# Kernel tuning notes

Measured on AMD Instinct MI355X. Metric: run time of the kernel, lower is better.

The kernel has to match this reference:

```python
import jax, jax.numpy as jnp
import numpy as np

G, NPG, K = 128, 1024, 16          # graphs, nodes per graph, kNN neighbors
NB_IN = 3
SLOPE = 0.01                        # torch.nn.LeakyReLU default negative_slope


def leaky(v):
    return jnp.where(v >= 0, v, SLOPE * v)


def knn_idx(pos, k):
    """pos: [G, n, 3] -> neighbor indices [G, n, k] within each graph, self excluded.
    Matches torch_geometric.nn.knn_graph (k nearest by Euclidean distance)."""
    sq = jnp.sum(pos * pos, axis=-1)                              # [G, n]
    d2 = sq[:, :, None] + sq[:, None, :] - 2.0 * jnp.einsum('gnd,gmd->gnm', pos, pos)
    n = pos.shape[1]
    d2 = d2 + jnp.eye(n, dtype=pos.dtype) * 1e9                   # exclude self-loops
    _, idx = jax.lax.top_k(-d2, k)                                # k smallest distances
    return idx


def edge_conv(h, idx, W1, b1, W2, b2):
    """EdgeConv with aggr='add': sum_j mlp(cat([x_i, x_j - x_i])).
    h: [G, n, F], idx: [G, n, k] -> [G, n, out]"""
    xj = jax.vmap(lambda hg, ig: hg[ig])(h, idx)                  # gather: [G, n, k, F]
    xi = jnp.broadcast_to(h[:, :, None, :], xj.shape)
    m = jnp.concatenate([xi, xj - xi], axis=-1)                   # [G, n, k, 2F]
    m = leaky(m @ W1 + b1)
    m = leaky(m @ W2 + b2)
    return jnp.sum(m, axis=2)                                     # scatter-add over k


def _linear_init(key, fin, fout):
    kw, kb = jax.random.split(key)
    lim = 1.0 / np.sqrt(fin)
    W = jax.random.uniform(kw, (fin, fout), jnp.float32, -lim, lim)
    b = jax.random.uniform(kb, (fout,), jnp.float32, -lim, lim)
    return W, b


def setup_inputs() -> dict:
    key = jax.random.key(0)
    ks = jax.random.split(key, 10)
    x = jax.random.normal(ks[0], (G * NPG, NB_IN), jnp.float32)
    batch = jnp.repeat(jnp.arange(G, dtype=jnp.int32), NPG)
    # layer 1 MLP: [2*3 -> 16 -> 16]; layer 2 MLP: [2*16 -> 16 -> 16]
    W1a, b1a = _linear_init(ks[1], 2 * NB_IN, 16)
    W2a, b2a = _linear_init(ks[2], 16, 16)
    W1b, b1b = _linear_init(ks[3], 2 * 16, 16)
    W2b, b2b = _linear_init(ks[4], 16, 16)
    # post-processing: [3+16+16=35 -> 16 -> 16]
    Wp1, bp1 = _linear_init(ks[5], 35, 16)
    Wp2, bp2 = _linear_init(ks[6], 16, 16)
    # readout: [16*3 poolings = 48 -> 128 -> 10]
    Wr1, br1 = _linear_init(ks[7], 48, 128)
    Wr2, br2 = _linear_init(ks[8], 128, 10)
    return {"x": x, "batch": batch,
            "W1a": W1a, "b1a": b1a, "W2a": W2a, "b2a": b2a,
            "W1b": W1b, "b1b": b1b, "W2b": W2b, "b2b": b2b,
            "Wp1": Wp1, "bp1": bp1, "Wp2": Wp2, "bp2": bp2,
            "Wr1": Wr1, "br1": br1, "Wr2": Wr2, "br2": br2}


def reference(x, batch, W1a, b1a, W2a, b2a, W1b, b1b, W2b, b2b,
              Wp1, bp1, Wp2, bp2, Wr1, br1, Wr2, br2):
    # equal-sized graphs sorted by batch id -> reshape to [G, n, F]
    h = x.reshape(G, NPG, -1)
    skips = [h]
    for (W1, b1, W2, b2) in ((W1a, b1a, W2a, b2a), (W1b, b1b, W2b, b2b)):
        idx = knn_idx(h[..., :3], K)       # features_subset = slice(0, 3)
        h = edge_conv(h, idx, W1, b1, W2, b2)
        skips.append(h)
    h = jnp.concatenate(skips, axis=-1)    # [G, n, 35]
    h = leaky(h @ Wp1 + bp1)
    h = leaky(h @ Wp2 + bp2)               # [G, n, 16]
    pooled = jnp.concatenate([h.min(axis=1), h.max(axis=1), h.mean(axis=1)], axis=-1)  # [G, 48]
    out = leaky(pooled @ Wr1 + br1) @ Wr2 + br2                   # [G, 10]
    return out
```

## Files before the change

### kernel.cpp

```cpp
#include <hip/hip_runtime.h>

#define NG 128
#define NN 1024
#define KK 16
#define PCAP 16
#define PMAX 23
#define SLOPE 0.01f
#define FINF 3.0e38f

typedef unsigned short u16;

__device__ __forceinline__ float leaky(float v) {
    return v >= 0.0f ? v : SLOPE * v;
}

__device__ __forceinline__ void sorted_insert(float (&bd)[KK], int (&bi)[KK],
                                              float d, int j) {
    bool c[KK];
#pragma unroll
    for (int t = 0; t < KK; ++t) c[t] = d < bd[t];
#pragma unroll
    for (int t = KK - 1; t >= 1; --t) {
        bd[t] = c[t] ? (c[t - 1] ? bd[t - 1] : d) : bd[t];
        bi[t] = c[t] ? (c[t - 1] ? bi[t - 1] : j) : bi[t];
    }
    bd[0] = c[0] ? d : bd[0];
    bi[0] = c[0] ? j : bi[0];
}

__device__ __forceinline__ void knn_scan(const float4* __restrict__ posq,
                                         float* __restrict__ pend_d,
                                         u16* __restrict__ pend_j,
                                         int tid, int i,
                                         u16* __restrict__ idx_out) {
    const float4 meq = posq[i];
    const float mex = -2.0f * meq.x, mey = -2.0f * meq.y, mez = -2.0f * meq.z;
    const float mew = meq.w;
    float bd[KK];
    int bi[KK];
#pragma unroll
    for (int t = 0; t < KK; ++t) { bd[t] = FINF; bi[t] = 0; }
    float T = FINF;
    int cnt = 0;

    for (int j0 = 0; j0 < NN; j0 += 8) {
        float4 p[8];
#pragma unroll
        for (int u = 0; u < 8; ++u) p[u] = posq[j0 + u];
#pragma unroll
        for (int u = 0; u < 8; ++u) {
            const int j = j0 + u;
            float d2 = fmaf(mex, p[u].x, fmaf(mey, p[u].y,
                          fmaf(mez, p[u].z, mew + p[u].w)));
            bool pass = (d2 < T) && (j != i);
            if (pass) {
                pend_d[tid + 256 * cnt] = d2;
                pend_j[tid + 256 * cnt] = (u16)j;
                ++cnt;
            }
        }
        if (__any(cnt >= PCAP)) {
#pragma unroll 1
            for (int s = 0; s < PMAX; ++s) {
                float d = (s < cnt) ? pend_d[tid + 256 * s] : FINF;
                int j = pend_j[tid + 256 * s];
                if (__any(d < bd[KK - 1])) sorted_insert(bd, bi, d, j);
            }
            cnt = 0;
            T = bd[KK - 1];
        }
    }
#pragma unroll 1
    for (int s = 0; s < PCAP; ++s) {
        float d = (s < cnt) ? pend_d[tid + 256 * s] : FINF;
        int j = pend_j[tid + 256 * s];
        if (__any(d < bd[KK - 1])) sorted_insert(bd, bi, d, j);
    }
#pragma unroll
    for (int t = 0; t < KK; ++t) idx_out[t] = (u16)bi[t];
}

__global__ __launch_bounds__(256) void knn1(
    const float* __restrict__ x, u16* __restrict__ idx)
{
    __shared__ float4 posq[NN];
    __shared__ float pend_d[256 * PMAX];
    __shared__ u16 pend_j[256 * PMAX];

    const int g = blockIdx.x >> 2;
    const int chunk = blockIdx.x & 3;
    const int tid = threadIdx.x;

    for (int n = tid; n < NN; n += 256) {
        const float* xp = x + (size_t)(g * NN + n) * 3;
        float px = xp[0], py = xp[1], pz = xp[2];
        posq[n] = make_float4(px, py, pz, px * px + py * py + pz * pz);
    }
    __syncthreads();

    const int i = chunk * 256 + tid;
    knn_scan(posq, pend_d, pend_j, tid, i, idx + (size_t)(g * NN + i) * KK);
}

__global__ __launch_bounds__(256) void knn2(
    const float* __restrict__ h1, u16* __restrict__ idx)
{
    __shared__ float4 posq[NN];
    __shared__ float pend_d[256 * PMAX];
    __shared__ u16 pend_j[256 * PMAX];

    const int g = blockIdx.x >> 2;
    const int chunk = blockIdx.x & 3;
    const int tid = threadIdx.x;

    for (int n = tid; n < NN; n += 256) {
        const float4 a = *(const float4*)(h1 + (size_t)(g * NN + n) * 16);
        posq[n] = make_float4(a.x, a.y, a.z, a.x * a.x + a.y * a.y + a.z * a.z);
    }
    __syncthreads();

    const int i = chunk * 256 + tid;
    knn_scan(posq, pend_d, pend_j, tid, i, idx + (size_t)(g * NN + i) * KK);
}

__device__ __forceinline__ void edge_pass(
    const float* __restrict__ u_lds,
    const float (&s1)[16],
    const u16* __restrict__ my_idx,
    const float* __restrict__ W2,
    const float* __restrict__ b2,
    float* __restrict__ out_row)
{
#pragma unroll 1
    for (int half = 0; half < 2; ++half) {
        float4 w2h[16][2];
#pragma unroll
        for (int f = 0; f < 16; ++f) {
            w2h[f][0] = *(const float4*)(W2 + f * 16 + half * 8);
            w2h[f][1] = *(const float4*)(W2 + f * 16 + half * 8 + 4);
        }
        float bb[8];
#pragma unroll
        for (int oo = 0; oo < 8; ++oo) bb[oo] = b2[half * 8 + oo];

        float acc[8];
#pragma unroll
        for (int oo = 0; oo < 8; ++oo) acc[oo] = 0.0f;

#pragma unroll 1
        for (int t = 0; t < KK; ++t) {
            const int j = my_idx[t];
            const float4* uj4 = (const float4*)(u_lds + j * 16);
            float4 u0 = uj4[0], u1 = uj4[1], u2 = uj4[2], u3 = uj4[3];
            float m1[16];
            m1[0]  = leaky(s1[0]  + u0.x);  m1[1]  = leaky(s1[1]  + u0.y);
            m1[2]  = leaky(s1[2]  + u0.z);  m1[3]  = leaky(s1[3]  + u0.w);
            m1[4]  = leaky(s1[4]  + u1.x);  m1[5]  = leaky(s1[5]  + u1.y);
            m1[6]  = leaky(s1[6]  + u1.z);  m1[7]  = leaky(s1[7]  + u1.w);
            m1[8]  = leaky(s1[8]  + u2.x);  m1[9]  = leaky(s1[9]  + u2.y);
            m1[10] = leaky(s1[10] + u2.z);  m1[11] = leaky(s1[11] + u2.w);
            m1[12] = leaky(s1[12] + u3.x);  m1[13] = leaky(s1[13] + u3.y);
            m1[14] = leaky(s1[14] + u3.z);  m1[15] = leaky(s1[15] + u3.w);

            float v[8];
#pragma unroll
            for (int oo = 0; oo < 8; ++oo) v[oo] = bb[oo];
#pragma unroll
            for (int f = 0; f < 16; ++f) {
                float4 wa = w2h[f][0], wb = w2h[f][1];
                v[0] += m1[f] * wa.x;  v[1] += m1[f] * wa.y;
                v[2] += m1[f] * wa.z;  v[3] += m1[f] * wa.w;
                v[4] += m1[f] * wb.x;  v[5] += m1[f] * wb.y;
                v[6] += m1[f] * wb.z;  v[7] += m1[f] * wb.w;
            }
#pragma unroll
            for (int oo = 0; oo < 8; ++oo) acc[oo] += leaky(v[oo]);
        }
        float4* o4 = (float4*)(out_row + half * 8);
        o4[0] = make_float4(acc[0], acc[1], acc[2], acc[3]);
        o4[1] = make_float4(acc[4], acc[5], acc[6], acc[7]);
    }
}

__global__ __launch_bounds__(256) void conv1(
    const float* __restrict__ x,
    const u16* __restrict__ idx,
    const float* __restrict__ W1,
    const float* __restrict__ b1,
    const float* __restrict__ W2,
    const float* __restrict__ b2,
    float* __restrict__ h1)
{
    __shared__ float u_lds[NN * 16];

    const int g = blockIdx.x >> 2;
    const int chunk = blockIdx.x & 3;
    const int tid = threadIdx.x;

    float wlo[3][16], whi[3][16];
#pragma unroll
    for (int c = 0; c < 3; ++c) {
#pragma unroll
        for (int q = 0; q < 4; ++q) {
            *(float4*)&wlo[c][q * 4] = *(const float4*)(W1 + c * 16 + q * 4);
            *(float4*)&whi[c][q * 4] = *(const float4*)(W1 + (3 + c) * 16 + q * 4);
        }
    }

#pragma unroll 1
    for (int r = 0; r < 4; ++r) {
        const int n = r * 256 + tid;
        const float* xp = x + ((size_t)g * NN + n) * 3;
        float px = xp[0], py = xp[1], pz = xp[2];
        float4* un = (float4*)(u_lds + n * 16);
#pragma unroll
        for (int q = 0; q < 4; ++q) {
            float4 uv;
            uv.x = px * whi[0][q * 4 + 0] + py * whi[1][q * 4 + 0] + pz * whi[2][q * 4 + 0];
            uv.y = px * whi[0][q * 4 + 1] + py * whi[1][q * 4 + 1] + pz * whi[2][q * 4 + 1];
            uv.z = px * whi[0][q * 4 + 2] + py * whi[1][q * 4 + 2] + pz * whi[2][q * 4 + 2];
            uv.w = px * whi[0][q * 4 + 3] + py * whi[1][q * 4 + 3] + pz * whi[2][q * 4 + 3];
            un[q] = uv;
        }
    }

    const int i = chunk * 256 + tid;
    const float* mp = x + ((size_t)g * NN + i) * 3;
    const float mxx = mp[0], myy = mp[1], mzz = mp[2];
    float s1[16];
#pragma unroll
    for (int o = 0; o < 16; ++o) {
        s1[o] = b1[o] + mxx * (wlo[0][o] - whi[0][o])
                      + myy * (wlo[1][o] - whi[1][o])
                      + mzz * (wlo[2][o] - whi[2][o]);
    }
    __syncthreads();

    edge_pass(u_lds, s1, idx + (size_t)(g * NN + i) * KK, W2, b2,
              h1 + (size_t)(g * NN + i) * 16);
}

__global__ __launch_bounds__(256) void conv2(
    const float* __restrict__ h1,
    const u16* __restrict__ idx,
    const float* __restrict__ W1,
    const float* __restrict__ b1,
    const float* __restrict__ W2,
    const float* __restrict__ b2,
    float* __restrict__ h2)
{
    __shared__ float tile[NN * 16];
    __shared__ float w1s[32 * 16];
    __shared__ float b1s[16];

    const int g = blockIdx.x >> 2;
    const int chunk = blockIdx.x & 3;
    const int tid = threadIdx.x;

    w1s[tid] = W1[tid];
    w1s[256 + tid] = W1[256 + tid];
    if (tid < 16) b1s[tid] = b1[tid];

    float4* t4 = (float4*)tile;
    const float4* src4 = (const float4*)(h1 + (size_t)g * NN * 16);
    for (int t = tid; t < NN * 4; t += 256) t4[t] = src4[t];
    __syncthreads();

    float s1[16];
#pragma unroll 1
    for (int r = 0; r < 4; ++r) {
        asm volatile("" ::: "memory");
        const int n = r * 256 + tid;
        float4 x0 = t4[n * 4 + 0], x1 = t4[n * 4 + 1];
        float4 x2 = t4[n * 4 + 2], x3 = t4[n * 4 + 3];
        float xr[16] = {x0.x, x0.y, x0.z, x0.w, x1.x, x1.y, x1.z, x1.w,
                        x2.x, x2.y, x2.z, x2.w, x3.x, x3.y, x3.z, x3.w};
        float uo[16];
#pragma unroll
        for (int og = 0; og < 4; ++og) {
            float a0 = 0.f, a1 = 0.f, a2 = 0.f, a3 = 0.f;
#pragma unroll
            for (int f = 0; f < 16; ++f) {
                float4 wv = *(const float4*)(w1s + (16 + f) * 16 + og * 4);
                a0 += xr[f] * wv.x; a1 += xr[f] * wv.y;
                a2 += xr[f] * wv.z; a3 += xr[f] * wv.w;
            }
            uo[og * 4 + 0] = a0; uo[og * 4 + 1] = a1;
            uo[og * 4 + 2] = a2; uo[og * 4 + 3] = a3;
        }
        if (r == chunk) {
            float t1[16];
#pragma unroll
            for (int og = 0; og < 4; ++og) {
                float a0 = 0.f, a1 = 0.f, a2 = 0.f, a3 = 0.f;
#pragma unroll
                for (int f = 0; f < 16; ++f) {
                    float4 wv = *(const float4*)(w1s + f * 16 + og * 4);
                    a0 += xr[f] * wv.x; a1 += xr[f] * wv.y;
                    a2 += xr[f] * wv.z; a3 += xr[f] * wv.w;
                }
                t1[og * 4 + 0] = a0; t1[og * 4 + 1] = a1;
                t1[og * 4 + 2] = a2; t1[og * 4 + 3] = a3;
            }
#pragma unroll
            for (int o = 0; o < 16; ++o) s1[o] = b1s[o] + t1[o] - uo[o];
        }
        t4[n * 4 + 0] = make_float4(uo[0], uo[1], uo[2], uo[3]);
        t4[n * 4 + 1] = make_float4(uo[4], uo[5], uo[6], uo[7]);
        t4[n * 4 + 2] = make_float4(uo[8], uo[9], uo[10], uo[11]);
        t4[n * 4 + 3] = make_float4(uo[12], uo[13], uo[14], uo[15]);
    }
    __syncthreads();

    const int i = chunk * 256 + tid;
    edge_pass(tile, s1, idx + (size_t)(g * NN + i) * KK, W2, b2,
              h2 + (size_t)(g * NN + i) * 16);
}

__global__ __launch_bounds__(256) void post_pool(
    const float* __restrict__ x,
    const float* __restrict__ h1,
    const float* __restrict__ h2,
    const float* __restrict__ Wp1, const float* __restrict__ bp1,
    const float* __restrict__ Wp2, const float* __restrict__ bp2,
    float* __restrict__ partial)
{
    __shared__ float wp1[35 * 16];
    __shared__ float wp2[16 * 16];
    __shared__ float sbp1[16], sbp2[16];
    __shared__ float red[3][4][16];

    const int g = blockIdx.x >> 2;
    const int chunk = blockIdx.x & 3;
    const int tid = threadIdx.x;

    wp2[tid] = Wp2[tid];
    for (int t = tid; t < 560; t += 256) wp1[t] = Wp1[t];
    if (tid < 16) { sbp1[tid] = bp1[tid]; sbp2[tid] = bp2[tid]; }
    __syncthreads();

    const int i = chunk * 256 + tid;
    const float* xp = x + (size_t)(g * NN + i) * 3;
    const float x0 = xp[0], x1 = xp[1], x2 = xp[2];
    const float4* p1v = (const float4*)(h1 + (size_t)(g * NN + i) * 16);
    float4 a0 = p1v[0], a1 = p1v[1], a2 = p1v[2], a3 = p1v[3];
    const float4* p2v = (const float4*)(h2 + (size_t)(g * NN + i) * 16);
    float4 c0 = p2v[0], c1 = p2v[1], c2 = p2v[2], c3 = p2v[3];

    float p1[16];
#pragma unroll
    for (int o = 0; o < 16; ++o) {
        float v = sbp1[o];
        v += x0 * wp1[0 * 16 + o];
        v += x1 * wp1[1 * 16 + o];
        v += x2 * wp1[2 * 16 + o];
        v += a0.x * wp1[3 * 16 + o];   v += a0.y * wp1[4 * 16 + o];
        v += a0.z * wp1[5 * 16 + o];   v += a0.w * wp1[6 * 16 + o];
        v += a1.x * wp1[7 * 16 + o];   v += a1.y * wp1[8 * 16 + o];
        v += a1.z * wp1[9 * 16 + o];   v += a1.w * wp1[10 * 16 + o];
        v += a2.x * wp1[11 * 16 + o];  v += a2.y * wp1[12 * 16 + o];
        v += a2.z * wp1[13 * 16 + o];  v += a2.w * wp1[14 * 16 + o];
        v += a3.x * wp1[15 * 16 + o];  v += a3.y * wp1[16 * 16 + o];
        v += a3.z * wp1[17 * 16 + o];  v += a3.w * wp1[18 * 16 + o];
        v += c0.x * wp1[19 * 16 + o];  v += c0.y * wp1[20 * 16 + o];
        v += c0.z * wp1[21 * 16 + o];  v += c0.w * wp1[22 * 16 + o];
        v += c1.x * wp1[23 * 16 + o];  v += c1.y * wp1[24 * 16 + o];
        v += c1.z * wp1[25 * 16 + o];  v += c1.w * wp1[26 * 16 + o];
        v += c2.x * wp1[27 * 16 + o];  v += c2.y * wp1[28 * 16 + o];
        v += c2.z * wp1[29 * 16 + o];  v += c2.w * wp1[30 * 16 + o];
        v += c3.x * wp1[31 * 16 + o];  v += c3.y * wp1[32 * 16 + o];
        v += c3.z * wp1[33 * 16 + o];  v += c3.w * wp1[34 * 16 + o];
        p1[o] = leaky(v);
    }

    float mn[16], mx[16], sm[16];
#pragma unroll
    for (int o = 0; o < 16; ++o) {
        float v = sbp2[o];
#pragma unroll
        for (int f = 0; f < 16; ++f) v += p1[f] * wp2[f * 16 + o];
        float p2 = leaky(v);
        mn[o] = p2; mx[o] = p2; sm[o] = p2;
    }

#pragma unroll
    for (int off = 32; off >= 1; off >>= 1) {
#pragma unroll
        for (int o = 0; o < 16; ++o) {
            mn[o] = fminf(mn[o], __shfl_xor(mn[o], off));
            mx[o] = fmaxf(mx[o], __shfl_xor(mx[o], off));
            sm[o] += __shfl_xor(sm[o], off);
        }
    }
    const int wave = tid >> 6;
    const int lane = tid & 63;
    if (lane == 0) {
#pragma unroll
        for (int o = 0; o < 16; ++o) {
            red[0][wave][o] = mn[o];
            red[1][wave][o] = mx[o];
            red[2][wave][o] = sm[o];
        }
    }
    __syncthreads();

    if (tid < 48) {
        const int stat = tid >> 4, o = tid & 15;
        float v;
        if (stat == 0)
            v = fminf(fminf(red[0][0][o], red[0][1][o]), fminf(red[0][2][o], red[0][3][o]));
        else if (stat == 1)
            v = fmaxf(fmaxf(red[1][0][o], red[1][1][o]), fmaxf(red[1][2][o], red[1][3][o]));
        else
            v = red[2][0][o] + red[2][1][o] + red[2][2][o] + red[2][3][o];
        partial[blockIdx.x * 48 + tid] = v;
    }
}

__global__ __launch_bounds__(128) void finalize(
    const float* __restrict__ partial,
    const float* __restrict__ Wr1, const float* __restrict__ br1,
    const float* __restrict__ Wr2, const float* __restrict__ br2,
    float* __restrict__ out)
{
    __shared__ float pooled[48];
    __shared__ float hidden[128];

    const int g = blockIdx.x;
    const int tid = threadIdx.x;

    if (tid < 48) {
        const int stat = tid >> 4;
        float a = partial[(g * 4 + 0) * 48 + tid];
        float b = partial[(g * 4 + 1) * 48 + tid];
        float c = partial[(g * 4 + 2) * 48 + tid];
        float d = partial[(g * 4 + 3) * 48 + tid];
        float v;
        if (stat == 0)      v = fminf(fminf(a, b), fminf(c, d));
        else if (stat == 1) v = fmaxf(fmaxf(a, b), fmaxf(c, d));
        else                v = (a + b + c + d) * (1.0f / NN);
        pooled[tid] = v;
    }
    __syncthreads();

    {
        float v = br1[tid];
#pragma unroll
        for (int f = 0; f < 48; ++f) v += pooled[f] * Wr1[f * 128 + tid];
        hidden[tid] = leaky(v);
    }
    __syncthreads();

    if (tid < 10) {
        float v = br2[tid];
#pragma unroll
        for (int f = 0; f < 128; ++f) v += hidden[f] * Wr2[f * 10 + tid];
        out[g * 10 + tid] = v;
    }
}

extern "C" void kernel_launch(void* const* d_in, const int* in_sizes, int n_in,
                              void* d_out, int out_size, void* d_ws, size_t ws_size,
                              hipStream_t stream) {
    const float* x   = (const float*)d_in[0];
    const float* W1a = (const float*)d_in[2];
    const float* b1a = (const float*)d_in[3];
    const float* W2a = (const float*)d_in[4];
    const float* b2a = (const float*)d_in[5];
    const float* W1b = (const float*)d_in[6];
    const float* b1b = (const float*)d_in[7];
    const float* W2b = (const float*)d_in[8];
    const float* b2b = (const float*)d_in[9];
    const float* Wp1 = (const float*)d_in[10];
    const float* bp1 = (const float*)d_in[11];
    const float* Wp2 = (const float*)d_in[12];
    const float* bp2 = (const float*)d_in[13];
    const float* Wr1 = (const float*)d_in[14];
    const float* br1 = (const float*)d_in[15];
    const float* Wr2 = (const float*)d_in[16];
    const float* br2 = (const float*)d_in[17];
    float* out = (float*)d_out;

    float* h1 = (float*)d_ws;
    float* h2 = h1 + (size_t)NG * NN * 16;
    u16* idx = (u16*)(h2 + (size_t)NG * NN * 16);
    float* partial = (float*)(idx + (size_t)NG * NN * KK);

    knn1<<<NG * 4, 256, 0, stream>>>(x, idx);
    conv1<<<NG * 4, 256, 0, stream>>>(x, idx, W1a, b1a, W2a, b2a, h1);
    knn2<<<NG * 4, 256, 0, stream>>>(h1, idx);
    conv2<<<NG * 4, 256, 0, stream>>>(h1, idx, W1b, b1b, W2b, b2b, h2);
    post_pool<<<NG * 4, 256, 0, stream>>>(x, h1, h2, Wp1, bp1, Wp2, bp2, partial);
    finalize<<<NG, 128, 0, stream>>>(partial, Wr1, br1, Wr2, br2, out);
}
```

Measured before the change: 550.1 us.

## Split kNN candidate scan across two threads per query and merge results

Each query point is now handled by two threads, each scanning half of the 1024 candidates and keeping its own top-16 list. The two sorted lists are merged through shared memory, and the result is written with vectorized 16-byte stores. Twice as many blocks are launched, which doubles parallelism, shortens each thread's serial scan and lowers the pending-buffer sizes and shared-memory use. The costs are the extra merge step, a block barrier, and more total insertion work because each half starts with a loose threshold.

```diff
diff --git a/kernel.cpp b/kernel.cpp
--- a/kernel.cpp
+++ b/kernel.cpp
@@ -3,8 +3,9 @@
 #define NG 128
 #define NN 1024
 #define KK 16
-#define PCAP 16
-#define PMAX 23
+#define HALF 512
+#define PCAP 8
+#define PMAX 16
 #define SLOPE 0.01f
 #define FINF 3.0e38f
 
@@ -28,22 +29,20 @@
     bi[0] = c[0] ? j : bi[0];
 }
 
-__device__ __forceinline__ void knn_scan(const float4* __restrict__ posq,
-                                         float* __restrict__ pend_d,
-                                         u16* __restrict__ pend_j,
-                                         int tid, int i,
-                                         u16* __restrict__ idx_out) {
+__device__ __forceinline__ void knn_scan_half(const float4* __restrict__ posq,
+                                              float* __restrict__ pend_d,
+                                              u16* __restrict__ pend_j,
+                                              int tid, int i, int jlo,
+                                              float (&bd)[KK], int (&bi)[KK]) {
     const float4 meq = posq[i];
     const float mex = -2.0f * meq.x, mey = -2.0f * meq.y, mez = -2.0f * meq.z;
     const float mew = meq.w;
-    float bd[KK];
-    int bi[KK];
 #pragma unroll
     for (int t = 0; t < KK; ++t) { bd[t] = FINF; bi[t] = 0; }
     float T = FINF;
     int cnt = 0;
 
-    for (int j0 = 0; j0 < NN; j0 += 8) {
+    for (int j0 = jlo; j0 < jlo + HALF; j0 += 8) {
         float4 p[8];
 #pragma unroll
         for (int u = 0; u < 8; ++u) p[u] = posq[j0 + u];
@@ -61,7 +60,7 @@
         }
         if (__any(cnt >= PCAP)) {
 #pragma unroll 1
-            for (int s = 0; s < PMAX; ++s) {
+            for (int s = 0; s < PMAX - 1; ++s) {
                 float d = (s < cnt) ? pend_d[tid + 256 * s] : FINF;
                 int j = pend_j[tid + 256 * s];
                 if (__any(d < bd[KK - 1])) sorted_insert(bd, bi, d, j);
@@ -76,19 +75,58 @@
         int j = pend_j[tid + 256 * s];
         if (__any(d < bd[KK - 1])) sorted_insert(bd, bi, d, j);
     }
-#pragma unroll
-    for (int t = 0; t < KK; ++t) idx_out[t] = (u16)bi[t];
+}
+
+__device__ __forceinline__ void knn_body(const float4* __restrict__ posq,
+                                         float* __restrict__ buf_d,
+                                         u16* __restrict__ buf_j,
+                                         int g, int chunk, int tid,
+                                         u16* __restrict__ idx) {
+    const int q = tid & 127;
+    const int half = tid >> 7;
+    const int i = chunk * 128 + q;
+
+    float bd[KK];
+    int bi[KK];
+    knn_scan_half(posq, buf_d, buf_j, tid, i, half * HALF, bd, bi);
+
+#pragma unroll
+    for (int t = 0; t < KK; ++t) {
+        buf_d[tid + 256 * t] = bd[t];
+        buf_j[tid + 256 * t] = (u16)bi[t];
+    }
+    __syncthreads();
+
+    if (tid < 128) {
+        int ia = 0, ib = 0;
+        unsigned int pack[8];
+#pragma unroll
+        for (int k = 0; k < KK; ++k) {
+            float da = buf_d[tid + 256 * ia];
+            float db = buf_d[(tid + 128) + 256 * ib];
+            bool ta = da <= db;
+            unsigned int j = ta ? (unsigned int)buf_j[tid + 256 * ia]
+                               : (unsigned int)buf_j[(tid + 128) + 256 * ib];
+            ia += ta ? 1 : 0;
+            ib += ta ? 0 : 1;
+            if ((k & 1) == 0) pack[k >> 1] = j;
+            else pack[k >> 1] |= j << 16;
+        }
+        uint4* o4 = (uint4*)(idx + ((size_t)g * NN + i) * KK);
+        o4[0] = make_uint4(pack[0], pack[1], pack[2], pack[3]);
+        o4[1] = make_uint4(pack[4], pack[5], pack[6], pack[7]);
+    }
 }
 
 __global__ __launch_bounds__(256) void knn1(
     const float* __restrict__ x, u16* __restrict__ idx)
 {
     __shared__ float4 posq[NN];
-    __shared__ float pend_d[256 * PMAX];
-    __shared__ u16 pend_j[256 * PMAX];
-
-    const int g = blockIdx.x >> 2;
-    const int chunk = blockIdx.x & 3;
+    __shared__ float buf_d[256 * PMAX];
+    __shared__ u16 buf_j[256 * PMAX];
+
+    const int g = blockIdx.x >> 3;
+    const int chunk = blockIdx.x & 7;
     const int tid = threadIdx.x;
 
     for (int n = tid; n < NN; n += 256) {
@@ -98,19 +136,18 @@
     }
     __syncthreads();
 
-    const int i = chunk * 256 + tid;
-    knn_scan(posq, pend_d, pend_j, tid, i, idx + (size_t)(g * NN + i) * KK);
+    knn_body(posq, buf_d, buf_j, g, chunk, tid, idx);
 }
 
 __global__ __launch_bounds__(256) void knn2(
     const float* __restrict__ h1, u16* __restrict__ idx)
 {
     __shared__ float4 posq[NN];
-    __shared__ float pend_d[256 * PMAX];
-    __shared__ u16 pend_j[256 * PMAX];
-
-    const int g = blockIdx.x >> 2;
-    const int chunk = blockIdx.x & 3;
+    __shared__ float buf_d[256 * PMAX];
+    __shared__ u16 buf_j[256 * PMAX];
+
+    const int g = blockIdx.x >> 3;
+    const int chunk = blockIdx.x & 7;
     const int tid = threadIdx.x;
 
     for (int n = tid; n < NN; n += 256) {
@@ -119,8 +156,7 @@
     }
     __syncthreads();
 
-    const int i = chunk * 256 + tid;
-    knn_scan(posq, pend_d, pend_j, tid, i, idx + (size_t)(g * NN + i) * KK);
+    knn_body(posq, buf_d, buf_j, g, chunk, tid, idx);
 }
 
 __device__ __forceinline__ void edge_pass(
@@ -486,9 +522,9 @@
     u16* idx = (u16*)(h2 + (size_t)NG * NN * 16);
     float* partial = (float*)(idx + (size_t)NG * NN * KK);
 
-    knn1<<<NG * 4, 256, 0, stream>>>(x, idx);
+    knn1<<<NG * 8, 256, 0, stream>>>(x, idx);
     conv1<<<NG * 4, 256, 0, stream>>>(x, idx, W1a, b1a, W2a, b2a, h1);
-    knn2<<<NG * 4, 256, 0, stream>>>(h1, idx);
+    knn2<<<NG * 8, 256, 0, stream>>>(h1, idx);
     conv2<<<NG * 4, 256, 0, stream>>>(h1, idx, W1b, b1b, W2b, b2b, h2);
     post_pool<<<NG * 4, 256, 0, stream>>>(x, h1, h2, Wp1, bp1, Wp2, bp2, partial);
     finalize<<<NG, 128, 0, stream>>>(partial, Wr1, br1, Wr2, br2, out);
```

Measured after the change: 572.6 us. 1.04x slower.
